# Performance work log

Measured on AMD Instinct MI355X. Metric: run time of the kernel, lower is better.

## Reference

```python
import jax, jax.numpy as jnp
import numpy as np
import math

B, NQ, NK = 8, 1024, 2048
DQ = DK = DV = 1024
H = 8
DH = DV // H
EPS = 1e-5


def _layernorm(x, g, b):
    mu = jnp.mean(x, axis=-1, keepdims=True)
    var = jnp.mean(jnp.square(x - mu), axis=-1, keepdims=True)
    return (x - mu) * jax.lax.rsqrt(var + EPS) * g + b


def setup_inputs() -> dict:
    key = jax.random.key(0)
    ks = jax.random.split(key, 12)
    s_q = 1.0 / math.sqrt(DQ)
    s_v = 1.0 / math.sqrt(DV)
    return {
        "Q": jax.random.normal(ks[0], (B, NQ, DQ), jnp.float32),
        "K": jax.random.normal(ks[1], (B, NK, DK), jnp.float32),
        "Wq": jax.random.normal(ks[2], (DQ, DV), jnp.float32) * s_q,
        "bq": jnp.zeros((DV,), jnp.float32),
        "Wk": jax.random.normal(ks[3], (DK, DV), jnp.float32) * s_q,
        "bk": jnp.zeros((DV,), jnp.float32),
        "Wv": jax.random.normal(ks[4], (DK, DV), jnp.float32) * s_q,
        "bv": jnp.zeros((DV,), jnp.float32),
        "Wo": jax.random.normal(ks[5], (DV, DV), jnp.float32) * s_v,
        "bo": jnp.zeros((DV,), jnp.float32),
        "g0": jnp.ones((DV,), jnp.float32),
        "b0": jnp.zeros((DV,), jnp.float32),
        "g1": jnp.ones((DV,), jnp.float32),
        "b1": jnp.zeros((DV,), jnp.float32),
    }


def reference(Q, K, Wq, bq, Wk, bk, Wv, bv, Wo, bo, g0, b0, g1, b1):
    # projections
    q = Q @ Wq + bq                      # [B, NQ, DV]
    k = K @ Wk + bk                      # [B, NK, DV]
    v = K @ Wv + bv                      # [B, NK, DV]
    qh = q.reshape(B, NQ, H, DH)
    kh = k.reshape(B, NK, H, DH)
    vh = v.reshape(B, NK, H, DH)
    # NOTE: original scales by sqrt(dim_V), not sqrt(d_head)
    scale = 1.0 / math.sqrt(DV)
    logits = jnp.einsum("bqhd,bkhd->bhqk", qh, kh) * scale
    A = jax.nn.softmax(logits, axis=-1)
    # residual baked into attention output: Q_ + A @ V_
    Oh = qh + jnp.einsum("bhqk,bkhd->bqhd", A, vh)
    O = Oh.reshape(B, NQ, DV)
    O = _layernorm(O, g0, b0)
    O = O + jax.nn.relu(O @ Wo + bo)
    O = _layernorm(O, g1, b1)
    return O
```

## Files before the change

### kernel.cpp

```cpp
#include <hip/hip_runtime.h>
#include <stdint.h>

#define DEVI static __device__ __forceinline__

typedef __attribute__((ext_vector_type(8))) short short8;
typedef __attribute__((ext_vector_type(4))) float floatx4;
typedef __attribute__((ext_vector_type(4))) unsigned short ushortx4;
typedef __attribute__((ext_vector_type(2))) long longx2;

DEVI unsigned short f2bf(float f) {
  union { float f; uint32_t u; } v; v.f = f;
  uint32_t r = v.u + 0x7FFFu + ((v.u >> 16) & 1u);
  return (unsigned short)(r >> 16);
}
DEVI unsigned short f2bf_trunc(float f) {
  union { float f; uint32_t u; } v; v.f = f;
  return (unsigned short)(v.u >> 16);
}
DEVI float bf2f(unsigned short s) {
  union { uint32_t u; float f; } v; v.u = ((uint32_t)s) << 16;
  return v.f;
}
DEVI uint32_t fbits(float f) {
  union { float f; uint32_t u; } v; v.f = f;
  return v.u;
}
DEVI unsigned char f2fp8(float f) {
  return (unsigned char)(__builtin_amdgcn_cvt_pk_fp8_f32(f, f, 0, false) & 0xff);
}
DEVI long pack8fp8(const short8 s) {
  int a = __builtin_amdgcn_cvt_pk_fp8_f32(bf2f((unsigned short)s[0]),
                                          bf2f((unsigned short)s[1]), 0, false);
  a = __builtin_amdgcn_cvt_pk_fp8_f32(bf2f((unsigned short)s[2]),
                                      bf2f((unsigned short)s[3]), a, true);
  int b = __builtin_amdgcn_cvt_pk_fp8_f32(bf2f((unsigned short)s[4]),
                                          bf2f((unsigned short)s[5]), 0, false);
  b = __builtin_amdgcn_cvt_pk_fp8_f32(bf2f((unsigned short)s[6]),
                                      bf2f((unsigned short)s[7]), b, true);
  union { int i[2]; long l; } u;
  u.i[0] = a; u.i[1] = b;
  return u.l;
}

DEVI void lds_cp16(void* lds, const void* g) {
  __builtin_amdgcn_global_load_lds(
      (const __attribute__((address_space(1))) uint32_t*)g,
      reinterpret_cast<__attribute__((address_space(3))) uint32_t*>(
          (uint32_t)reinterpret_cast<uintptr_t>(lds)),
      16, 0, 0);
}

__global__ __launch_bounds__(256) void cvt_qk(const float* __restrict__ Q,
                                              const float* __restrict__ K,
                                              unsigned short* __restrict__ Qb,
                                              unsigned char* __restrict__ Kf8) {
  const int bid = blockIdx.x;
  if (bid < 8192) {
    const size_t i = (size_t)bid * 256 + threadIdx.x;
    const floatx4 v = ((const floatx4*)Q)[i];
    ushortx4 o;
    o.x = f2bf(v.x); o.y = f2bf(v.y); o.z = f2bf(v.z); o.w = f2bf(v.w);
    ((ushortx4*)Qb)[i] = o;
  } else {
    const size_t i = (size_t)(bid - 8192) * 256 + threadIdx.x;
    const floatx4 v = ((const floatx4*)K)[i];
    int p = __builtin_amdgcn_cvt_pk_fp8_f32(v.x, v.y, 0, false);
    p = __builtin_amdgcn_cvt_pk_fp8_f32(v.z, v.w, p, true);
    ((int*)Kf8)[i] = p;
  }
}

__global__ __launch_bounds__(256) void wtrans4(const float* __restrict__ Wq,
                                               const float* __restrict__ Wk,
                                               const float* __restrict__ Wv,
                                               const float* __restrict__ Wo,
                                               unsigned short* __restrict__ Wt,
                                               unsigned char* __restrict__ Wt8) {
  __shared__ float t[32][33];
  const int tx = threadIdx.x, ty = threadIdx.y;
  const int z = blockIdx.z;
  const float* W = (z == 0) ? Wq : (z == 1) ? Wk : (z == 2) ? Wv : Wo;
  const int c0 = blockIdx.x * 32, r0 = blockIdx.y * 32;
#pragma unroll
  for (int i = 0; i < 4; i++)
    t[ty + i * 8][tx] = W[(size_t)(r0 + ty + i * 8) * 1024 + c0 + tx];
  __syncthreads();
  if (z == 0 || z == 3) {
    unsigned short* D = Wt + (z == 0 ? 0 : (size_t)1024 * 1024);
#pragma unroll
    for (int i = 0; i < 4; i++)
      D[(size_t)(c0 + ty + i * 8) * 1024 + r0 + tx] = f2bf(t[tx][ty + i * 8]);
  } else {
    unsigned char* D = Wt8 + (z == 1 ? 0 : (size_t)1024 * 1024);
#pragma unroll
    for (int i = 0; i < 4; i++)
      D[(size_t)(c0 + ty + i * 8) * 1024 + r0 + tx] = f2fp8(t[tx][ty + i * 8]);
  }
}

template <int EPI>
__global__ __launch_bounds__(256, 3) void gemm_bt(
    const unsigned short* __restrict__ A, const unsigned short* __restrict__ Bt,
    const float* __restrict__ bias, const unsigned short* __restrict__ X1,
    void* __restrict__ Cout) {
  __shared__ unsigned short As[2][4][128][8];
  __shared__ unsigned short Bs[2][4][128][8];

  const int tid = threadIdx.x;
  const int lane = tid & 63, w = tid >> 6;
  const int wr = w >> 1, wc = w & 1;
  const int qd = lane >> 4, l16 = lane & 15;
  const int bid = blockIdx.x;
  const int xcd = bid & 7, loc = bid >> 3;
  const int m0 = (xcd * 8 + (loc & 7)) * 128;
  const int n0 = (loc >> 3) * 128;

  floatx4 acc[4][4];
#pragma unroll
  for (int i = 0; i < 4; i++)
#pragma unroll
    for (int j = 0; j < 4; j++) { floatx4 z = {0.f, 0.f, 0.f, 0.f}; acc[i][j] = z; }

  const int prow = tid & 127;
  const unsigned short* aptr = A + (size_t)(m0 + prow) * 1024 + ((tid >> 7) << 3);
  const unsigned short* bptr = Bt + (size_t)(n0 + prow) * 1024 + ((tid >> 7) << 3);
  const int dstoff = tid * 8;

  lds_cp16(&As[0][0][0][0] + dstoff, aptr);
  lds_cp16(&As[0][0][0][0] + dstoff + 2048, aptr + 16);
  lds_cp16(&Bs[0][0][0][0] + dstoff, bptr);
  lds_cp16(&Bs[0][0][0][0] + dstoff + 2048, bptr + 16);

  for (int it = 0; it < 32; it++) {
    __syncthreads();
    if (it < 31) {
      const int nb = (it + 1) & 1, k0 = (it + 1) * 32;
      lds_cp16(&As[nb][0][0][0] + dstoff, aptr + k0);
      lds_cp16(&As[nb][0][0][0] + dstoff + 2048, aptr + k0 + 16);
      lds_cp16(&Bs[nb][0][0][0] + dstoff, bptr + k0);
      lds_cp16(&Bs[nb][0][0][0] + dstoff + 2048, bptr + k0 + 16);
    }
    const int cur = it & 1;
    short8 af[4], bf[4];
#pragma unroll
    for (int mi = 0; mi < 4; mi++)
      af[mi] = *(const short8*)&As[cur][qd][wr * 64 + mi * 16 + l16][0];
#pragma unroll
    for (int ni = 0; ni < 4; ni++)
      bf[ni] = *(const short8*)&Bs[cur][qd][wc * 64 + ni * 16 + l16][0];
#pragma unroll
    for (int mi = 0; mi < 4; mi++)
#pragma unroll
      for (int ni = 0; ni < 4; ni++)
        acc[mi][ni] =
            __builtin_amdgcn_mfma_f32_16x16x32_bf16(af[mi], bf[ni], acc[mi][ni], 0, 0, 0);
  }

#pragma unroll
  for (int mi = 0; mi < 4; mi++) {
#pragma unroll
    for (int ni = 0; ni < 4; ni++) {
      const int row = m0 + wr * 64 + mi * 16 + qd * 4;
      const int col = n0 + wc * 64 + ni * 16 + l16;
      const float bv = bias[col];
      if constexpr (EPI == 0) {
        unsigned short* C = (unsigned short*)Cout;
#pragma unroll
        for (int r = 0; r < 4; r++)
          C[(size_t)(row + r) * 1024 + col] = f2bf(acc[mi][ni][r] + bv);
      } else {
        unsigned short* C = (unsigned short*)Cout;
#pragma unroll
        for (int r = 0; r < 4; r++) {
          const float x1 = bf2f(X1[(size_t)(row + r) * 1024 + col]);
          C[(size_t)(row + r) * 1024 + col] = f2bf(x1 + fmaxf(acc[mi][ni][r] + bv, 0.f));
        }
      }
    }
  }
}

__global__ __launch_bounds__(256, 3) void gemm_kv_f8(
    const unsigned char* __restrict__ A, const unsigned char* __restrict__ Bt,
    const float* __restrict__ biasK, const float* __restrict__ biasV,
    unsigned char* __restrict__ CK8, unsigned char* __restrict__ CV8) {
  __shared__ unsigned char As[2][4][128][16];
  __shared__ unsigned char Bs[2][4][128][16];

  const int tid = threadIdx.x;
  const int lane = tid & 63, w = tid >> 6;
  const int wr = w >> 1, wc = w & 1;
  const int qd = lane >> 4, l16 = lane & 15;
  const int bid = blockIdx.x;
  const int xcd = bid & 7, loc = bid >> 3;
  const int m0 = (xcd * 16 + (loc & 15)) * 128;
  const int n0 = (loc >> 4) * 128;

  floatx4 acc[4][4];
#pragma unroll
  for (int i = 0; i < 4; i++)
#pragma unroll
    for (int j = 0; j < 4; j++) { floatx4 z = {0.f, 0.f, 0.f, 0.f}; acc[i][j] = z; }

  const int srow = tid & 127, sc = tid >> 7;
  const unsigned char* aptr = A + (size_t)(m0 + srow) * 1024 + sc * 16;
  const unsigned char* bptr = Bt + (size_t)(n0 + srow) * 1024 + sc * 16;
  unsigned char* dA = &As[0][sc][srow][0];
  unsigned char* dB = &Bs[0][sc][srow][0];

  lds_cp16(dA, aptr);
  lds_cp16(dA + 4096, aptr + 32);
  lds_cp16(dB, bptr);
  lds_cp16(dB + 4096, bptr + 32);

  for (int it = 0; it < 16; it++) {
    __syncthreads();
    if (it < 15) {
      const int nb = (it + 1) & 1, k0 = (it + 1) * 64;
      lds_cp16(dA + nb * 8192, aptr + k0);
      lds_cp16(dA + nb * 8192 + 4096, aptr + k0 + 32);
      lds_cp16(dB + nb * 8192, bptr + k0);
      lds_cp16(dB + nb * 8192 + 4096, bptr + k0 + 32);
    }
    const int cur = it & 1;
    longx2 av[4], bvv[4];
#pragma unroll
    for (int mi = 0; mi < 4; mi++) {
      const int row = wr * 64 + mi * 16 + l16;
      av[mi] = *(const longx2*)&As[cur][qd][row][0];
    }
#pragma unroll
    for (int ni = 0; ni < 4; ni++) {
      const int row = wc * 64 + ni * 16 + l16;
      bvv[ni] = *(const longx2*)&Bs[cur][qd][row][0];
    }
#pragma unroll
    for (int mi = 0; mi < 4; mi++)
#pragma unroll
      for (int ni = 0; ni < 4; ni++)
        acc[mi][ni] = __builtin_amdgcn_mfma_f32_16x16x32_fp8_fp8(
            av[mi].x, bvv[ni].x, acc[mi][ni], 0, 0, 0);
#pragma unroll
    for (int mi = 0; mi < 4; mi++)
#pragma unroll
      for (int ni = 0; ni < 4; ni++)
        acc[mi][ni] = __builtin_amdgcn_mfma_f32_16x16x32_fp8_fp8(
            av[mi].y, bvv[ni].y, acc[mi][ni], 0, 0, 0);
  }

#pragma unroll
  for (int mi = 0; mi < 4; mi++) {
#pragma unroll
    for (int ni = 0; ni < 4; ni++) {
      const int row = m0 + wr * 64 + mi * 16 + qd * 4;
      const int col = n0 + wc * 64 + ni * 16 + l16;
      if (col < 1024) {
        const float bv = biasK[col];
#pragma unroll
        for (int r = 0; r < 4; r++)
          CK8[(size_t)(row + r) * 1024 + col] = f2fp8(acc[mi][ni][r] + bv);
      } else {
        const int vc = col - 1024;
        const float bv = biasV[vc];
        const int bb = row >> 11, nk = row & 2047;
        const int hh = vc >> 7, dh = vc & 127;
        int p = __builtin_amdgcn_cvt_pk_fp8_f32(acc[mi][ni][0] + bv,
                                                acc[mi][ni][1] + bv, 0, false);
        p = __builtin_amdgcn_cvt_pk_fp8_f32(acc[mi][ni][2] + bv,
                                            acc[mi][ni][3] + bv, p, true);
        *(uint32_t*)&CV8[((((size_t)(bb * 8 + hh)) * 256 + (nk >> 3)) * 128 + dh) * 8 +
                         (nk & 7)] = (uint32_t)p;
      }
    }
  }
}

__global__ __launch_bounds__(256, 3) void attn(
    const unsigned short* __restrict__ qb, const unsigned char* __restrict__ kb8,
    const unsigned char* __restrict__ vt8, unsigned short* __restrict__ Ob) {
  __shared__ __align__(16) unsigned char smc[32768];
  unsigned short* sm16 = (unsigned short*)smc;

  const int tid = threadIdx.x;
  const int lane = tid & 63, w = tid >> 6;
  const int qd = lane >> 4, l16 = lane & 15;
  const int bid = blockIdx.x;
  const int qt = bid >> 6, bh = bid & 63;
  const int h = bh >> 3, b = bh & 7;
  const int m0 = qt * 128;

  const size_t qbase = ((size_t)(b * 1024 + m0)) * 1024 + h * 128;
  const size_t kbase8 = ((size_t)(b * 2048)) * 1024 + h * 128;
  const size_t vbase8 = (size_t)(b * 8 + h) * 262144;

#pragma unroll
  for (int i = 0; i < 8; i++) {
    const int p = i * 256 + tid;
    const int row = p & 127, c = p >> 7;
    lds_cp16(&sm16[c * 1024 + row * 8], qb + qbase + (size_t)row * 1024 + c * 8);
  }
  __syncthreads();
  long qx[2][2], qy[2][2];
#pragma unroll
  for (int p = 0; p < 2; p++)
#pragma unroll
    for (int nt = 0; nt < 2; nt++) {
      const int row = w * 32 + nt * 16 + l16;
      const short8 qa = *(const short8*)&sm16[(p * 8 + qd * 2) * 1024 + row * 8];
      const short8 qc = *(const short8*)&sm16[(p * 8 + qd * 2 + 1) * 1024 + row * 8];
      qx[p][nt] = pack8fp8(qa);
      qy[p][nt] = pack8fp8(qc);
    }
  __syncthreads();

  {
    const int kr = tid >> 3, sl = tid & 7;
    lds_cp16(smc + tid * 16,
             kb8 + kbase8 + (size_t)kr * 1024 + (sl ^ (kr & 7)) * 16);
    lds_cp16(smc + 8192 + tid * 16,
             vt8 + vbase8 + (size_t)(tid >> 6) * 1024 + (tid & 63) * 16);
  }

  floatx4 oacc[8][2];
#pragma unroll
  for (int mt = 0; mt < 8; mt++)
#pragma unroll
    for (int nt = 0; nt < 2; nt++) { floatx4 z = {0.f, 0.f, 0.f, 0.f}; oacc[mt][nt] = z; }
  float lsum[2] = {0.f, 0.f};

  const int addrLo = ((qd & 1) * 32 + l16) * 4;
  const int addrHi = addrLo + 64;
  const bool loHalf = (lane < 32);

  for (int it = 0; it < 64; it++) {
    __syncthreads();
    if (it + 1 < 64) {
      const int nb = (it + 1) & 1, kv0 = (it + 1) * 32;
      const int kr = tid >> 3, sl = tid & 7;
      lds_cp16(smc + nb * 4096 + tid * 16,
               kb8 + kbase8 + (size_t)(kv0 + kr) * 1024 + (sl ^ (kr & 7)) * 16);
      lds_cp16(smc + 8192 + nb * 4096 + tid * 16,
               vt8 + vbase8 + (size_t)kv0 * 128 + (tid >> 6) * 1024 + (tid & 63) * 16);
    }
    const int cur = it & 1;

    floatx4 st[2][2];
#pragma unroll
    for (int mt = 0; mt < 2; mt++)
#pragma unroll
      for (int nt = 0; nt < 2; nt++) { floatx4 z = {0.f, 0.f, 0.f, 0.f}; st[mt][nt] = z; }
    __builtin_amdgcn_s_setprio(1);
#pragma unroll
    for (int p = 0; p < 2; p++) {
#pragma unroll
      for (int mt = 0; mt < 2; mt++) {
        const longx2 kk = *(const longx2*)(smc + cur * 4096 + (mt * 16 + l16) * 128 +
                                           (((p * 4 + qd) ^ (l16 & 7)) << 4));
        st[mt][0] = __builtin_amdgcn_mfma_f32_16x16x32_fp8_fp8(kk.x, qx[p][0], st[mt][0], 0, 0, 0);
        st[mt][1] = __builtin_amdgcn_mfma_f32_16x16x32_fp8_fp8(kk.x, qx[p][1], st[mt][1], 0, 0, 0);
        st[mt][0] = __builtin_amdgcn_mfma_f32_16x16x32_fp8_fp8(kk.y, qy[p][0], st[mt][0], 0, 0, 0);
        st[mt][1] = __builtin_amdgcn_mfma_f32_16x16x32_fp8_fp8(kk.y, qy[p][1], st[mt][1], 0, 0, 0);
      }
    }
    __builtin_amdgcn_s_setprio(0);

    long vl[8];
#pragma unroll
    for (int mt = 0; mt < 8; mt++)
      vl[mt] = *(const long*)(smc + 8192 + cur * 4096 + qd * 1024 + (mt * 16 + l16) * 8);

    uint32_t pkf[2][2];
#pragma unroll
    for (int mt = 0; mt < 2; mt++)
#pragma unroll
      for (int nt = 0; nt < 2; nt++) {
        const float e0 = __expf(st[mt][nt][0] * 0.03125f);
        const float e1 = __expf(st[mt][nt][1] * 0.03125f);
        const float e2 = __expf(st[mt][nt][2] * 0.03125f);
        const float e3 = __expf(st[mt][nt][3] * 0.03125f);
        lsum[nt] += (e0 + e1) + (e2 + e3);
        int p = __builtin_amdgcn_cvt_pk_fp8_f32(e0, e1, 0, false);
        p = __builtin_amdgcn_cvt_pk_fp8_f32(e2, e3, p, true);
        pkf[mt][nt] = (uint32_t)p;
      }

#pragma unroll
    for (int nt = 0; nt < 2; nt++) {
      int lo0 = __builtin_amdgcn_ds_bpermute(addrLo, (int)pkf[0][nt]);
      int lo1 = __builtin_amdgcn_ds_bpermute(addrLo, (int)pkf[1][nt]);
      int hi0 = __builtin_amdgcn_ds_bpermute(addrHi, (int)pkf[0][nt]);
      int hi1 = __builtin_amdgcn_ds_bpermute(addrHi, (int)pkf[1][nt]);
      union { int i[2]; long l; } u;
      u.i[0] = loHalf ? lo0 : lo1;
      u.i[1] = loHalf ? hi0 : hi1;
      const long pfl = u.l;
      __builtin_amdgcn_s_setprio(1);
#pragma unroll
      for (int mt = 0; mt < 8; mt++)
        oacc[mt][nt] =
            __builtin_amdgcn_mfma_f32_16x16x32_fp8_fp8(vl[mt], pfl, oacc[mt][nt], 0, 0, 0);
      __builtin_amdgcn_s_setprio(0);
    }
  }

  float inv[2];
#pragma unroll
  for (int nt = 0; nt < 2; nt++) {
    float s = lsum[nt];
    s += __shfl_xor(s, 16);
    s += __shfl_xor(s, 32);
    inv[nt] = 1.f / s;
  }

  __syncthreads();
#pragma unroll
  for (int mt = 0; mt < 8; mt++)
#pragma unroll
    for (int nt = 0; nt < 2; nt++) {
      const int q = w * 32 + nt * 16 + l16;
#pragma unroll
      for (int r = 0; r < 4; r++) {
        const int dh = mt * 16 + qd * 4 + r;
        const int c = dh >> 3, off = dh & 7;
        sm16[q * 128 + ((c ^ (q & 15)) * 8) + off] = f2bf_trunc(oacc[mt][nt][r] * inv[nt]);
      }
    }
  __syncthreads();
#pragma unroll
  for (int i = 0; i < 8; i++) {
    const int p = i * 256 + tid;
    const int row = p >> 4, c = p & 15;
    const short8 ov = *(const short8*)&sm16[row * 128 + ((c ^ (row & 15)) * 8)];
    const short8 qres = *(const short8*)(qb + qbase + (size_t)row * 1024 + c * 8);
    union { unsigned short us[8]; short8 s; } o;
#pragma unroll
    for (int e = 0; e < 8; e++)
      o.us[e] = f2bf(bf2f((unsigned short)ov[e]) + bf2f((unsigned short)qres[e]));
    *(short8*)(Ob + qbase + (size_t)row * 1024 + c * 8) = o.s;
  }
}

__global__ __launch_bounds__(256) void ln_rows(const unsigned short* __restrict__ X,
                                               const float* __restrict__ g,
                                               const float* __restrict__ bb,
                                               unsigned short* __restrict__ Y) {
  __shared__ float red[8];
  const int row = blockIdx.x, tid = threadIdx.x;
  const int w = tid >> 6, lane = tid & 63;
  const ushortx4 u = ((const ushortx4*)(X + (size_t)row * 1024))[tid];
  float x0 = bf2f(u.x), x1 = bf2f(u.y), x2 = bf2f(u.z), x3 = bf2f(u.w);
  float s = x0 + x1 + x2 + x3;
  float s2 = x0 * x0 + x1 * x1 + x2 * x2 + x3 * x3;
#pragma unroll
  for (int off = 1; off < 64; off <<= 1) { s += __shfl_xor(s, off); s2 += __shfl_xor(s2, off); }
  if (lane == 0) { red[w] = s; red[4 + w] = s2; }
  __syncthreads();
  s = red[0] + red[1] + red[2] + red[3];
  s2 = red[4] + red[5] + red[6] + red[7];
  const float mu = s * (1.f / 1024.f);
  const float rs = rsqrtf(s2 * (1.f / 1024.f) - mu * mu + 1e-5f);
  const floatx4 gv = ((const floatx4*)g)[tid];
  const floatx4 bv = ((const floatx4*)bb)[tid];
  ushortx4 o;
  o.x = f2bf((x0 - mu) * rs * gv.x + bv.x);
  o.y = f2bf((x1 - mu) * rs * gv.y + bv.y);
  o.z = f2bf((x2 - mu) * rs * gv.z + bv.z);
  o.w = f2bf((x3 - mu) * rs * gv.w + bv.w);
  ((ushortx4*)(Y + (size_t)row * 1024))[tid] = o;
}

__global__ __launch_bounds__(256) void ln_b2f(const unsigned short* __restrict__ X,
                                              const float* __restrict__ g,
                                              const float* __restrict__ bb,
                                              float* __restrict__ out) {
  __shared__ float red[8];
  const int row = blockIdx.x, tid = threadIdx.x;
  const int w = tid >> 6, lane = tid & 63;
  const ushortx4 u = ((const ushortx4*)(X + (size_t)row * 1024))[tid];
  float x0 = bf2f(u.x), x1 = bf2f(u.y), x2 = bf2f(u.z), x3 = bf2f(u.w);
  float s = x0 + x1 + x2 + x3;
  float s2 = x0 * x0 + x1 * x1 + x2 * x2 + x3 * x3;
#pragma unroll
  for (int off = 1; off < 64; off <<= 1) { s += __shfl_xor(s, off); s2 += __shfl_xor(s2, off); }
  if (lane == 0) { red[w] = s; red[4 + w] = s2; }
  __syncthreads();
  s = red[0] + red[1] + red[2] + red[3];
  s2 = red[4] + red[5] + red[6] + red[7];
  const float mu = s * (1.f / 1024.f);
  const float rs = rsqrtf(s2 * (1.f / 1024.f) - mu * mu + 1e-5f);
  const floatx4 gv = ((const floatx4*)g)[tid];
  const floatx4 bv = ((const floatx4*)bb)[tid];
  floatx4 o;
  o.x = (x0 - mu) * rs * gv.x + bv.x;
  o.y = (x1 - mu) * rs * gv.y + bv.y;
  o.z = (x2 - mu) * rs * gv.z + bv.z;
  o.w = (x3 - mu) * rs * gv.w + bv.w;
  ((floatx4*)(out + (size_t)row * 1024))[tid] = o;
}

extern "C" void kernel_launch(void* const* d_in, const int* in_sizes, int n_in,
                              void* d_out, int out_size, void* d_ws, size_t ws_size,
                              hipStream_t stream) {
  (void)in_sizes; (void)n_in; (void)out_size; (void)ws_size;
  const float* Q  = (const float*)d_in[0];
  const float* K  = (const float*)d_in[1];
  const float* Wq = (const float*)d_in[2];
  const float* bq = (const float*)d_in[3];
  const float* Wk = (const float*)d_in[4];
  const float* bk = (const float*)d_in[5];
  const float* Wv = (const float*)d_in[6];
  const float* bv = (const float*)d_in[7];
  const float* Wo = (const float*)d_in[8];
  const float* bo = (const float*)d_in[9];
  const float* g0 = (const float*)d_in[10];
  const float* b0 = (const float*)d_in[11];
  const float* g1 = (const float*)d_in[12];
  const float* b1 = (const float*)d_in[13];
  float* out = (float*)d_out;

  char* ws = (char*)d_ws;
  const size_t MB = 1u << 20;
  unsigned short* Qb  = (unsigned short*)(ws + 0);
  unsigned short* X1  = (unsigned short*)(ws + 16 * MB);
  unsigned short* Wt  = (unsigned short*)(ws + 32 * MB);
  unsigned char*  Wt8 = (unsigned char*)(ws + 36 * MB);
  unsigned char*  Kf8 = (unsigned char*)(ws + 38 * MB);
  unsigned short* qbp = (unsigned short*)(ws + 54 * MB);
  unsigned char*  kb8p = (unsigned char*)(ws + 70 * MB);
  unsigned char*  vt8 = (unsigned char*)(ws + 102 * MB);
  unsigned short* O   = Qb;
  unsigned short* O2b = (unsigned short*)(ws + 70 * MB);

  unsigned short* Wqt = Wt;
  unsigned short* Wot = Wt + (size_t)1024 * 1024;

  cvt_qk<<<24576, 256, 0, stream>>>(Q, K, Qb, Kf8);
  wtrans4<<<dim3(32, 32, 4), dim3(32, 8), 0, stream>>>(Wq, Wk, Wv, Wo, Wt, Wt8);

  gemm_bt<0><<<512, 256, 0, stream>>>(Qb, Wqt, bq, nullptr, qbp);
  gemm_kv_f8<<<2048, 256, 0, stream>>>(Kf8, Wt8, bk, bv, kb8p, vt8);
  attn<<<512, 256, 0, stream>>>(qbp, kb8p, vt8, O);
  ln_rows<<<8192, 256, 0, stream>>>(O, g0, b0, X1);
  gemm_bt<2><<<512, 256, 0, stream>>>(X1, Wot, bo, X1, O2b);
  ln_b2f<<<8192, 256, 0, stream>>>(O2b, g1, b1, out);
}
```

Before: 407.9 us.

## Fuse fp32-to-bf16/fp8 input conversion into Q and KV projection GEMM loads

Removes the separate cvt_qk pass. The Q and KV projection GEMMs now load fp32 activations directly into registers, convert them (bf16 by truncation, fp8 via packed cvt), and store them into LDS after the MFMA step. This saves a full read/write pass over Q and K plus one launch. The cost is more global traffic per tile, since fp32 rows are re-read across column tiles, and register-staged loads in place of async LDS copies. It also switches Q rounding to truncation.

```diff
diff --git a/kernel.cpp b/kernel.cpp
--- a/kernel.cpp
+++ b/kernel.cpp
@@ -7,6 +7,7 @@
 typedef __attribute__((ext_vector_type(4))) float floatx4;
 typedef __attribute__((ext_vector_type(4))) unsigned short ushortx4;
 typedef __attribute__((ext_vector_type(2))) long longx2;
+typedef __attribute__((ext_vector_type(4))) uint32_t uintx4;
 
 DEVI unsigned short f2bf(float f) {
   union { float f; uint32_t u; } v; v.f = f;
@@ -41,6 +42,26 @@
   u.i[0] = a; u.i[1] = b;
   return u.l;
 }
+DEVI short8 pack8bf(floatx4 a, floatx4 b) {
+  union { uint32_t u[4]; short8 s; } r;
+  r.u[0] = __builtin_amdgcn_perm(fbits(a.y), fbits(a.x), 0x07060302);
+  r.u[1] = __builtin_amdgcn_perm(fbits(a.w), fbits(a.z), 0x07060302);
+  r.u[2] = __builtin_amdgcn_perm(fbits(b.y), fbits(b.x), 0x07060302);
+  r.u[3] = __builtin_amdgcn_perm(fbits(b.w), fbits(b.z), 0x07060302);
+  return r.s;
+}
+DEVI uintx4 pack16f8(floatx4 a, floatx4 b, floatx4 c, floatx4 d) {
+  uintx4 r;
+  int p = __builtin_amdgcn_cvt_pk_fp8_f32(a.x, a.y, 0, false);
+  r.x = (uint32_t)__builtin_amdgcn_cvt_pk_fp8_f32(a.z, a.w, p, true);
+  p = __builtin_amdgcn_cvt_pk_fp8_f32(b.x, b.y, 0, false);
+  r.y = (uint32_t)__builtin_amdgcn_cvt_pk_fp8_f32(b.z, b.w, p, true);
+  p = __builtin_amdgcn_cvt_pk_fp8_f32(c.x, c.y, 0, false);
+  r.z = (uint32_t)__builtin_amdgcn_cvt_pk_fp8_f32(c.z, c.w, p, true);
+  p = __builtin_amdgcn_cvt_pk_fp8_f32(d.x, d.y, 0, false);
+  r.w = (uint32_t)__builtin_amdgcn_cvt_pk_fp8_f32(d.z, d.w, p, true);
+  return r;
+}
 
 DEVI void lds_cp16(void* lds, const void* g) {
   __builtin_amdgcn_global_load_lds(
@@ -48,26 +69,6 @@
       reinterpret_cast<__attribute__((address_space(3))) uint32_t*>(
           (uint32_t)reinterpret_cast<uintptr_t>(lds)),
       16, 0, 0);
-}
-
-__global__ __launch_bounds__(256) void cvt_qk(const float* __restrict__ Q,
-                                              const float* __restrict__ K,
-                                              unsigned short* __restrict__ Qb,
-                                              unsigned char* __restrict__ Kf8) {
-  const int bid = blockIdx.x;
-  if (bid < 8192) {
-    const size_t i = (size_t)bid * 256 + threadIdx.x;
-    const floatx4 v = ((const floatx4*)Q)[i];
-    ushortx4 o;
-    o.x = f2bf(v.x); o.y = f2bf(v.y); o.z = f2bf(v.z); o.w = f2bf(v.w);
-    ((ushortx4*)Qb)[i] = o;
-  } else {
-    const size_t i = (size_t)(bid - 8192) * 256 + threadIdx.x;
-    const floatx4 v = ((const floatx4*)K)[i];
-    int p = __builtin_amdgcn_cvt_pk_fp8_f32(v.x, v.y, 0, false);
-    p = __builtin_amdgcn_cvt_pk_fp8_f32(v.z, v.w, p, true);
-    ((int*)Kf8)[i] = p;
-  }
 }
 
 __global__ __launch_bounds__(256) void wtrans4(const float* __restrict__ Wq,
@@ -98,11 +99,9 @@
   }
 }
 
-template <int EPI>
-__global__ __launch_bounds__(256, 3) void gemm_bt(
-    const unsigned short* __restrict__ A, const unsigned short* __restrict__ Bt,
-    const float* __restrict__ bias, const unsigned short* __restrict__ X1,
-    void* __restrict__ Cout) {
+__global__ __launch_bounds__(256, 3) void gemm_q_f32(
+    const float* __restrict__ Af, const unsigned short* __restrict__ Bt,
+    const float* __restrict__ bias, unsigned short* __restrict__ Cout) {
   __shared__ unsigned short As[2][4][128][8];
   __shared__ unsigned short Bs[2][4][128][8];
 
@@ -122,6 +121,93 @@
     for (int j = 0; j < 4; j++) { floatx4 z = {0.f, 0.f, 0.f, 0.f}; acc[i][j] = z; }
 
   const int prow = tid & 127;
+  const float* af = Af + (size_t)(m0 + prow) * 1024 + ((tid >> 7) << 3);
+  const unsigned short* bptr = Bt + (size_t)(n0 + prow) * 1024 + ((tid >> 7) << 3);
+  const int dstoff = tid * 8;
+  unsigned short* dA = &As[0][0][0][0];
+  unsigned short* dB = &Bs[0][0][0][0];
+
+  {
+    const floatx4 a0 = *(const floatx4*)(af + 0);
+    const floatx4 a1 = *(const floatx4*)(af + 4);
+    const floatx4 a2 = *(const floatx4*)(af + 16);
+    const floatx4 a3 = *(const floatx4*)(af + 20);
+    *(short8*)(dA + dstoff) = pack8bf(a0, a1);
+    *(short8*)(dA + dstoff + 2048) = pack8bf(a2, a3);
+    lds_cp16(dB + dstoff, bptr);
+    lds_cp16(dB + dstoff + 2048, bptr + 16);
+  }
+
+  for (int it = 0; it < 32; it++) {
+    __syncthreads();
+    floatx4 a0, a1, a2, a3;
+    const int nb = (it + 1) & 1;
+    if (it < 31) {
+      const int k0 = (it + 1) * 32;
+      a0 = *(const floatx4*)(af + k0);
+      a1 = *(const floatx4*)(af + k0 + 4);
+      a2 = *(const floatx4*)(af + k0 + 16);
+      a3 = *(const floatx4*)(af + k0 + 20);
+      lds_cp16(dB + nb * 4096 + dstoff, bptr + k0);
+      lds_cp16(dB + nb * 4096 + dstoff + 2048, bptr + k0 + 16);
+    }
+    const int cur = it & 1;
+    short8 afr[4], bfr[4];
+#pragma unroll
+    for (int mi = 0; mi < 4; mi++)
+      afr[mi] = *(const short8*)&As[cur][qd][wr * 64 + mi * 16 + l16][0];
+#pragma unroll
+    for (int ni = 0; ni < 4; ni++)
+      bfr[ni] = *(const short8*)&Bs[cur][qd][wc * 64 + ni * 16 + l16][0];
+#pragma unroll
+    for (int mi = 0; mi < 4; mi++)
+#pragma unroll
+      for (int ni = 0; ni < 4; ni++)
+        acc[mi][ni] =
+            __builtin_amdgcn_mfma_f32_16x16x32_bf16(afr[mi], bfr[ni], acc[mi][ni], 0, 0, 0);
+    if (it < 31) {
+      *(short8*)(dA + nb * 4096 + dstoff) = pack8bf(a0, a1);
+      *(short8*)(dA + nb * 4096 + dstoff + 2048) = pack8bf(a2, a3);
+    }
+  }
+
+#pragma unroll
+  for (int mi = 0; mi < 4; mi++) {
+#pragma unroll
+    for (int ni = 0; ni < 4; ni++) {
+      const int row = m0 + wr * 64 + mi * 16 + qd * 4;
+      const int col = n0 + wc * 64 + ni * 16 + l16;
+      const float bv = bias[col];
+#pragma unroll
+      for (int r = 0; r < 4; r++)
+        Cout[(size_t)(row + r) * 1024 + col] = f2bf(acc[mi][ni][r] + bv);
+    }
+  }
+}
+
+__global__ __launch_bounds__(256, 3) void gemm_wo(
+    const unsigned short* __restrict__ A, const unsigned short* __restrict__ Bt,
+    const float* __restrict__ bias, const unsigned short* __restrict__ X1,
+    unsigned short* __restrict__ Cout) {
+  __shared__ unsigned short As[2][4][128][8];
+  __shared__ unsigned short Bs[2][4][128][8];
+
+  const int tid = threadIdx.x;
+  const int lane = tid & 63, w = tid >> 6;
+  const int wr = w >> 1, wc = w & 1;
+  const int qd = lane >> 4, l16 = lane & 15;
+  const int bid = blockIdx.x;
+  const int xcd = bid & 7, loc = bid >> 3;
+  const int m0 = (xcd * 8 + (loc & 7)) * 128;
+  const int n0 = (loc >> 3) * 128;
+
+  floatx4 acc[4][4];
+#pragma unroll
+  for (int i = 0; i < 4; i++)
+#pragma unroll
+    for (int j = 0; j < 4; j++) { floatx4 z = {0.f, 0.f, 0.f, 0.f}; acc[i][j] = z; }
+
+  const int prow = tid & 127;
   const unsigned short* aptr = A + (size_t)(m0 + prow) * 1024 + ((tid >> 7) << 3);
   const unsigned short* bptr = Bt + (size_t)(n0 + prow) * 1024 + ((tid >> 7) << 3);
   const int dstoff = tid * 8;
@@ -163,25 +249,17 @@
       const int row = m0 + wr * 64 + mi * 16 + qd * 4;
       const int col = n0 + wc * 64 + ni * 16 + l16;
       const float bv = bias[col];
-      if constexpr (EPI == 0) {
-        unsigned short* C = (unsigned short*)Cout;
-#pragma unroll
-        for (int r = 0; r < 4; r++)
-          C[(size_t)(row + r) * 1024 + col] = f2bf(acc[mi][ni][r] + bv);
-      } else {
-        unsigned short* C = (unsigned short*)Cout;
-#pragma unroll
-        for (int r = 0; r < 4; r++) {
-          const float x1 = bf2f(X1[(size_t)(row + r) * 1024 + col]);
-          C[(size_t)(row + r) * 1024 + col] = f2bf(x1 + fmaxf(acc[mi][ni][r] + bv, 0.f));
-        }
+#pragma unroll
+      for (int r = 0; r < 4; r++) {
+        const float x1 = bf2f(X1[(size_t)(row + r) * 1024 + col]);
+        Cout[(size_t)(row + r) * 1024 + col] = f2bf(x1 + fmaxf(acc[mi][ni][r] + bv, 0.f));
       }
     }
   }
 }
 
 __global__ __launch_bounds__(256, 3) void gemm_kv_f8(
-    const unsigned char* __restrict__ A, const unsigned char* __restrict__ Bt,
+    const float* __restrict__ Kf, const unsigned char* __restrict__ Bt,
     const float* __restrict__ biasK, const float* __restrict__ biasV,
     unsigned char* __restrict__ CK8, unsigned char* __restrict__ CV8) {
   __shared__ unsigned char As[2][4][128][16];
@@ -203,22 +281,40 @@
     for (int j = 0; j < 4; j++) { floatx4 z = {0.f, 0.f, 0.f, 0.f}; acc[i][j] = z; }
 
   const int srow = tid & 127, sc = tid >> 7;
-  const unsigned char* aptr = A + (size_t)(m0 + srow) * 1024 + sc * 16;
+  const float* af = Kf + (size_t)(m0 + srow) * 1024 + sc * 16;
   const unsigned char* bptr = Bt + (size_t)(n0 + srow) * 1024 + sc * 16;
   unsigned char* dA = &As[0][sc][srow][0];
   unsigned char* dB = &Bs[0][sc][srow][0];
 
-  lds_cp16(dA, aptr);
-  lds_cp16(dA + 4096, aptr + 32);
-  lds_cp16(dB, bptr);
-  lds_cp16(dB + 4096, bptr + 32);
+  {
+    const floatx4 a0 = *(const floatx4*)(af + 0);
+    const floatx4 a1 = *(const floatx4*)(af + 4);
+    const floatx4 a2 = *(const floatx4*)(af + 8);
+    const floatx4 a3 = *(const floatx4*)(af + 12);
+    const floatx4 a4 = *(const floatx4*)(af + 32);
+    const floatx4 a5 = *(const floatx4*)(af + 36);
+    const floatx4 a6 = *(const floatx4*)(af + 40);
+    const floatx4 a7 = *(const floatx4*)(af + 44);
+    *(uintx4*)dA = pack16f8(a0, a1, a2, a3);
+    *(uintx4*)(dA + 4096) = pack16f8(a4, a5, a6, a7);
+    lds_cp16(dB, bptr);
+    lds_cp16(dB + 4096, bptr + 32);
+  }
 
   for (int it = 0; it < 16; it++) {
     __syncthreads();
+    floatx4 a0, a1, a2, a3, a4, a5, a6, a7;
+    const int nb = (it + 1) & 1;
     if (it < 15) {
-      const int nb = (it + 1) & 1, k0 = (it + 1) * 64;
-      lds_cp16(dA + nb * 8192, aptr + k0);
-      lds_cp16(dA + nb * 8192 + 4096, aptr + k0 + 32);
+      const int k0 = (it + 1) * 64;
+      a0 = *(const floatx4*)(af + k0);
+      a1 = *(const floatx4*)(af + k0 + 4);
+      a2 = *(const floatx4*)(af + k0 + 8);
+      a3 = *(const floatx4*)(af + k0 + 12);
+      a4 = *(const floatx4*)(af + k0 + 32);
+      a5 = *(const floatx4*)(af + k0 + 36);
+      a6 = *(const floatx4*)(af + k0 + 40);
+      a7 = *(const floatx4*)(af + k0 + 44);
       lds_cp16(dB + nb * 8192, bptr + k0);
       lds_cp16(dB + nb * 8192 + 4096, bptr + k0 + 32);
     }
@@ -246,6 +342,10 @@
       for (int ni = 0; ni < 4; ni++)
         acc[mi][ni] = __builtin_amdgcn_mfma_f32_16x16x32_fp8_fp8(
             av[mi].y, bvv[ni].y, acc[mi][ni], 0, 0, 0);
+    if (it < 15) {
+      *(uintx4*)(dA + nb * 8192) = pack16f8(a0, a1, a2, a3);
+      *(uintx4*)(dA + nb * 8192 + 4096) = pack16f8(a4, a5, a6, a7);
+    }
   }
 
 #pragma unroll
@@ -520,27 +620,24 @@
 
   char* ws = (char*)d_ws;
   const size_t MB = 1u << 20;
-  unsigned short* Qb  = (unsigned short*)(ws + 0);
   unsigned short* X1  = (unsigned short*)(ws + 16 * MB);
   unsigned short* Wt  = (unsigned short*)(ws + 32 * MB);
   unsigned char*  Wt8 = (unsigned char*)(ws + 36 * MB);
-  unsigned char*  Kf8 = (unsigned char*)(ws + 38 * MB);
   unsigned short* qbp = (unsigned short*)(ws + 54 * MB);
   unsigned char*  kb8p = (unsigned char*)(ws + 70 * MB);
   unsigned char*  vt8 = (unsigned char*)(ws + 102 * MB);
-  unsigned short* O   = Qb;
+  unsigned short* O   = (unsigned short*)(ws + 0);
   unsigned short* O2b = (unsigned short*)(ws + 70 * MB);
 
   unsigned short* Wqt = Wt;
   unsigned short* Wot = Wt + (size_t)1024 * 1024;
 
-  cvt_qk<<<24576, 256, 0, stream>>>(Q, K, Qb, Kf8);
   wtrans4<<<dim3(32, 32, 4), dim3(32, 8), 0, stream>>>(Wq, Wk, Wv, Wo, Wt, Wt8);
 
-  gemm_bt<0><<<512, 256, 0, stream>>>(Qb, Wqt, bq, nullptr, qbp);
-  gemm_kv_f8<<<2048, 256, 0, stream>>>(Kf8, Wt8, bk, bv, kb8p, vt8);
+  gemm_q_f32<<<512, 256, 0, stream>>>(Q, Wqt, bq, qbp);
+  gemm_kv_f8<<<2048, 256, 0, stream>>>(K, Wt8, bk, bv, kb8p, vt8);
   attn<<<512, 256, 0, stream>>>(qbp, kb8p, vt8, O);
   ln_rows<<<8192, 256, 0, stream>>>(O, g0, b0, X1);
-  gemm_bt<2><<<512, 256, 0, stream>>>(X1, Wot, bo, X1, O2b);
+  gemm_wo<<<512, 256, 0, stream>>>(X1, Wot, bo, X1, O2b);
   ln_b2f<<<8192, 256, 0, stream>>>(O2b, g1, b1, out);
 }
```

Measured after the change: 512.3 us. 1.26x slower.

## Use scaled 16x16x128 FP8 MFMA with 128-wide K tiles in KV projection GEMM

Applied to the files above, without the earlier changes.

Replaces the pair of 16x16x32 FP8 MFMA calls per K-step in the fused K/V projection GEMM with a single MX-scaled 16x16x128 f8f6f4 MFMA, using a unit scale. The K tile per iteration doubles to 128, so there are half as many loop trips and barriers. LDS buffers double and launch bounds drop from 3 to 2 blocks per SM. The aim is higher MFMA throughput and less per-iteration overhead, at the cost of occupancy and a different operand lane layout that must match the instruction's expected K ordering.

```diff
diff --git a/kernel.cpp b/kernel.cpp
--- a/kernel.cpp
+++ b/kernel.cpp
@@ -7,6 +7,8 @@
 typedef __attribute__((ext_vector_type(4))) float floatx4;
 typedef __attribute__((ext_vector_type(4))) unsigned short ushortx4;
 typedef __attribute__((ext_vector_type(2))) long longx2;
+typedef __attribute__((ext_vector_type(4))) uint32_t uintx4;
+typedef __attribute__((ext_vector_type(8))) int intx8;
 
 DEVI unsigned short f2bf(float f) {
   union { float f; uint32_t u; } v; v.f = f;
@@ -180,12 +182,12 @@
   }
 }
 
-__global__ __launch_bounds__(256, 3) void gemm_kv_f8(
+__global__ __launch_bounds__(256, 2) void gemm_kv_f8(
     const unsigned char* __restrict__ A, const unsigned char* __restrict__ Bt,
     const float* __restrict__ biasK, const float* __restrict__ biasV,
     unsigned char* __restrict__ CK8, unsigned char* __restrict__ CV8) {
-  __shared__ unsigned char As[2][4][128][16];
-  __shared__ unsigned char Bs[2][4][128][16];
+  __shared__ unsigned char As[2][8][128][16];
+  __shared__ unsigned char Bs[2][8][128][16];
 
   const int tid = threadIdx.x;
   const int lane = tid & 63, w = tid >> 6;
@@ -208,44 +210,50 @@
   unsigned char* dA = &As[0][sc][srow][0];
   unsigned char* dB = &Bs[0][sc][srow][0];
 
-  lds_cp16(dA, aptr);
-  lds_cp16(dA + 4096, aptr + 32);
-  lds_cp16(dB, bptr);
-  lds_cp16(dB + 4096, bptr + 32);
-
-  for (int it = 0; it < 16; it++) {
+#pragma unroll
+  for (int j = 0; j < 4; j++) {
+    lds_cp16(dA + j * 4096, aptr + j * 32);
+    lds_cp16(dB + j * 4096, bptr + j * 32);
+  }
+
+  const int SCL = 0x7F7F7F7F;
+
+  for (int it = 0; it < 8; it++) {
     __syncthreads();
-    if (it < 15) {
-      const int nb = (it + 1) & 1, k0 = (it + 1) * 64;
-      lds_cp16(dA + nb * 8192, aptr + k0);
-      lds_cp16(dA + nb * 8192 + 4096, aptr + k0 + 32);
-      lds_cp16(dB + nb * 8192, bptr + k0);
-      lds_cp16(dB + nb * 8192 + 4096, bptr + k0 + 32);
+    if (it < 7) {
+      const int nb = (it + 1) & 1, k0 = (it + 1) * 128;
+#pragma unroll
+      for (int j = 0; j < 4; j++) {
+        lds_cp16(dA + nb * 16384 + j * 4096, aptr + k0 + j * 32);
+        lds_cp16(dB + nb * 16384 + j * 4096, bptr + k0 + j * 32);
+      }
     }
     const int cur = it & 1;
-    longx2 av[4], bvv[4];
+    intx8 av[4], bvv[4];
 #pragma unroll
     for (int mi = 0; mi < 4; mi++) {
       const int row = wr * 64 + mi * 16 + l16;
-      av[mi] = *(const longx2*)&As[cur][qd][row][0];
+      const uintx4 lo = *(const uintx4*)&As[cur][2 * qd][row][0];
+      const uintx4 hi = *(const uintx4*)&As[cur][2 * qd + 1][row][0];
+      union { uintx4 q[2]; intx8 v; } u;
+      u.q[0] = lo; u.q[1] = hi;
+      av[mi] = u.v;
     }
 #pragma unroll
     for (int ni = 0; ni < 4; ni++) {
       const int row = wc * 64 + ni * 16 + l16;
-      bvv[ni] = *(const longx2*)&Bs[cur][qd][row][0];
+      const uintx4 lo = *(const uintx4*)&Bs[cur][2 * qd][row][0];
+      const uintx4 hi = *(const uintx4*)&Bs[cur][2 * qd + 1][row][0];
+      union { uintx4 q[2]; intx8 v; } u;
+      u.q[0] = lo; u.q[1] = hi;
+      bvv[ni] = u.v;
     }
 #pragma unroll
     for (int mi = 0; mi < 4; mi++)
 #pragma unroll
       for (int ni = 0; ni < 4; ni++)
-        acc[mi][ni] = __builtin_amdgcn_mfma_f32_16x16x32_fp8_fp8(
-            av[mi].x, bvv[ni].x, acc[mi][ni], 0, 0, 0);
-#pragma unroll
-    for (int mi = 0; mi < 4; mi++)
-#pragma unroll
-      for (int ni = 0; ni < 4; ni++)
-        acc[mi][ni] = __builtin_amdgcn_mfma_f32_16x16x32_fp8_fp8(
-            av[mi].y, bvv[ni].y, acc[mi][ni], 0, 0, 0);
+        acc[mi][ni] = __builtin_amdgcn_mfma_scale_f32_16x16x128_f8f6f4(
+            av[mi], bvv[ni], acc[mi][ni], 0, 0, 0, SCL, 0, SCL);
   }
 
 #pragma unroll
```

After: 753.6 us. 84.8% more time.
